# Optimization experiments

Hardware: AMD Instinct MI355X
Metric: run time of the kernel (lower is better)

The kernel has to match this reference:

```python
import jax, jax.numpy as jnp
import numpy as np

N = 100000   # nodes
E = 1600000  # edges (avg degree 16)
D = 64       # feature dim
STEPS = 3

def setup_inputs() -> dict:
    key = jax.random.key(0)
    ks = jax.random.split(key, 16)
    def rn(i, shape, scale=1.0):
        return jax.random.normal(ks[i], shape, dtype=jnp.float32) * scale
    inp = {
        "nodes": rn(0, (N, D)),
        "edges": rn(1, (E, D)),
        "globals_": rn(2, (1, D)),
        "senders": jax.random.randint(ks[3], (E,), 0, N, dtype=jnp.int32),
        "receivers": jax.random.randint(ks[4], (E,), 0, N, dtype=jnp.int32),
        # edge MLP: in 4*D -> D -> D
        "We1": rn(5, (4 * D, D), (4 * D) ** -0.5),
        "be1": jnp.zeros((D,), jnp.float32),
        "We2": rn(6, (D, D), D ** -0.5),
        "be2": jnp.zeros((D,), jnp.float32),
        # node MLP: in 3*D -> D -> D
        "Wn1": rn(7, (3 * D, D), (3 * D) ** -0.5),
        "bn1": jnp.zeros((D,), jnp.float32),
        "Wn2": rn(8, (D, D), D ** -0.5),
        "bn2": jnp.zeros((D,), jnp.float32),
        # global MLP: in 3*D -> D -> D
        "Wg1": rn(9, (3 * D, D), (3 * D) ** -0.5),
        "bg1": jnp.zeros((D,), jnp.float32),
        "Wg2": rn(10, (D, D), D ** -0.5),
        "bg2": jnp.zeros((D,), jnp.float32),
    }
    return inp

def _mlp(x, W1, b1, W2, b2):
    return jax.nn.relu(x @ W1 + b1) @ W2 + b2

def reference(nodes, edges, globals_, senders, receivers,
              We1, be1, We2, be2, Wn1, bn1, Wn2, bn2, Wg1, bg1, Wg2, bg2):
    g = globals_  # [1, D], single graph
    n_nodes = nodes.shape[0]
    for _ in range(STEPS):
        # --- edge update: gather sender/receiver node feats + broadcast globals ---
        sent = nodes[senders]        # [E, D]
        recv = nodes[receivers]      # [E, D]
        ge = jnp.broadcast_to(g, (edges.shape[0], g.shape[-1]))
        edges = _mlp(jnp.concatenate([edges, sent, recv, ge], axis=-1),
                     We1, be1, We2, be2)  # [E, D]
        # --- aggregate edges to nodes (received messages) ---
        received = jax.ops.segment_sum(edges, receivers, num_segments=n_nodes)
        gn = jnp.broadcast_to(g, (n_nodes, g.shape[-1]))
        nodes = _mlp(jnp.concatenate([nodes, received, gn], axis=-1),
                     Wn1, bn1, Wn2, bn2)  # [N, D]
        # --- aggregate to globals (single graph => full sums) ---
        agg_n = jnp.sum(nodes, axis=0, keepdims=True)  # [1, D]
        agg_e = jnp.sum(edges, axis=0, keepdims=True)  # [1, D]
        g = _mlp(jnp.concatenate([agg_n, agg_e, g], axis=-1),
                 Wg1, bg1, Wg2, bg2)  # [1, D]
    return nodes, edges, g
```

## Files before the change

kernel.cpp:

```cpp
#include <hip/hip_runtime.h>

#define DD 64
typedef unsigned int uint32;
typedef unsigned short ushort16;
typedef short bf16x8 __attribute__((ext_vector_type(8)));
typedef float f32x4 __attribute__((ext_vector_type(4)));

__device__ __forceinline__ ushort16 f2bf(float x) {
    uint32 u = __float_as_uint(x);
    uint32 r = (u + 0x7FFFu + ((u >> 16) & 1u)) >> 16;
    return (ushort16)r;
}
__device__ __forceinline__ float bf2f(ushort16 h) {
    return __uint_as_float(((uint32)h) << 16);
}

__device__ __forceinline__ void split8f(const float4& a, const float4& b, bf16x8& ah, bf16x8& al) {
    float xs[8] = {a.x, a.y, a.z, a.w, b.x, b.y, b.z, b.w};
#pragma unroll
    for (int i = 0; i < 8; ++i) {
        ushort16 hi = f2bf(xs[i]);
        ah[i] = (short)hi;
        al[i] = (short)f2bf(xs[i] - bf2f(hi));
    }
}

__device__ __forceinline__ void mfma_ks(const unsigned short* __restrict__ wks, int l,
                                        const bf16x8* ah, const bf16x8* al, f32x4 (*acc)[4]) {
#pragma unroll
    for (int tt = 0; tt < 4; ++tt) {
        bf16x8 bh = *(const bf16x8*)(wks + ((size_t)(tt * 2 + 0) * 64 + l) * 8);
        bf16x8 bl = *(const bf16x8*)(wks + ((size_t)(tt * 2 + 1) * 64 + l) * 8);
#pragma unroll
        for (int m = 0; m < 4; ++m) {
            acc[m][tt] = __builtin_amdgcn_mfma_f32_16x16x32_bf16(ah[m], bh, acc[m][tt], 0, 0, 0);
            acc[m][tt] = __builtin_amdgcn_mfma_f32_16x16x32_bf16(ah[m], bl, acc[m][tt], 0, 0, 0);
            acc[m][tt] = __builtin_amdgcn_mfma_f32_16x16x32_bf16(al[m], bh, acc[m][tt], 0, 0, 0);
        }
    }
}
__device__ __forceinline__ void mfma_ks_hi(const unsigned short* __restrict__ wks, int l,
                                           const bf16x8* ah, f32x4 (*acc)[4]) {
#pragma unroll
    for (int tt = 0; tt < 4; ++tt) {
        bf16x8 bh = *(const bf16x8*)(wks + ((size_t)(tt * 2 + 0) * 64 + l) * 8);
        bf16x8 bl = *(const bf16x8*)(wks + ((size_t)(tt * 2 + 1) * 64 + l) * 8);
#pragma unroll
        for (int m = 0; m < 4; ++m) {
            acc[m][tt] = __builtin_amdgcn_mfma_f32_16x16x32_bf16(ah[m], bh, acc[m][tt], 0, 0, 0);
            acc[m][tt] = __builtin_amdgcn_mfma_f32_16x16x32_bf16(ah[m], bl, acc[m][tt], 0, 0, 0);
        }
    }
}
__device__ __forceinline__ void mfma_ks1(const unsigned short* __restrict__ wks, int l,
                                         bf16x8 ah, bf16x8 al, f32x4* acc) {
#pragma unroll
    for (int tt = 0; tt < 4; ++tt) {
        bf16x8 bh = *(const bf16x8*)(wks + ((size_t)(tt * 2 + 0) * 64 + l) * 8);
        bf16x8 bl = *(const bf16x8*)(wks + ((size_t)(tt * 2 + 1) * 64 + l) * 8);
        acc[tt] = __builtin_amdgcn_mfma_f32_16x16x32_bf16(ah, bh, acc[tt], 0, 0, 0);
        acc[tt] = __builtin_amdgcn_mfma_f32_16x16x32_bf16(ah, bl, acc[tt], 0, 0, 0);
        acc[tt] = __builtin_amdgcn_mfma_f32_16x16x32_bf16(al, bh, acc[tt], 0, 0, 0);
    }
}

__global__ void zero_counts_kernel(int* __restrict__ counts, int N) {
    int i = blockIdx.x * blockDim.x + threadIdx.x;
    if (i < N) counts[i] = 0;
}
__global__ void hist_kernel(const int* __restrict__ recv, int* __restrict__ counts, int E) {
    int i = blockIdx.x * blockDim.x + threadIdx.x;
    if (i < E) atomicAdd(&counts[recv[i]], 1);
}
__global__ __launch_bounds__(1024) void scan_kernel(const int* __restrict__ counts,
                                                    int* __restrict__ offs,
                                                    int* __restrict__ cursor, int N) {
    __shared__ int sm[1024];
    __shared__ int carryS;
    int t = threadIdx.x;
    if (t == 0) carryS = 0;
    __syncthreads();
    for (int base = 0; base < N; base += 4096) {
        int idx = base + t * 4;
        int x0 = (idx + 0 < N) ? counts[idx + 0] : 0;
        int x1 = (idx + 1 < N) ? counts[idx + 1] : 0;
        int x2 = (idx + 2 < N) ? counts[idx + 2] : 0;
        int x3 = (idx + 3 < N) ? counts[idx + 3] : 0;
        int s1 = x0 + x1, s2 = s1 + x2, s3 = s2 + x3;
        sm[t] = s3;
        __syncthreads();
        for (int d = 1; d < 1024; d <<= 1) {
            int v = (t >= d) ? sm[t - d] : 0;
            __syncthreads();
            sm[t] += v;
            __syncthreads();
        }
        int excl = sm[t] - s3 + carryS;
        if (idx < N)     { offs[idx]     = excl;      cursor[idx]     = excl; }
        if (idx + 1 < N) { offs[idx + 1] = excl + x0; cursor[idx + 1] = excl + x0; }
        if (idx + 2 < N) { offs[idx + 2] = excl + s1; cursor[idx + 2] = excl + s1; }
        if (idx + 3 < N) { offs[idx + 3] = excl + s2; cursor[idx + 3] = excl + s2; }
        int chunkTotal = sm[1023];
        __syncthreads();
        if (t == 0) carryS += chunkTotal;
        __syncthreads();
    }
    if (t == 0) offs[N] = carryS;
}
__global__ void scatter_kernel(const int* __restrict__ recv, int* __restrict__ cursor,
                               int* __restrict__ perm, int* __restrict__ inv, int E) {
    int i = blockIdx.x * blockDim.x + threadIdx.x;
    if (i < E) {
        int p = atomicAdd(&cursor[recv[i]], 1);
        perm[p] = i;
        inv[i] = p;
    }
}

__global__ void prep_bias_kernel(const float* __restrict__ g,
                                 const float* __restrict__ We1, const float* __restrict__ be1,
                                 const float* __restrict__ Wn1, const float* __restrict__ bn1,
                                 float* __restrict__ be1e, float* __restrict__ bn1e) {
    int j = threadIdx.x;
    float a = be1[j];
    float b = bn1[j];
    for (int k = 0; k < DD; ++k) {
        float gk = g[k];
        a = fmaf(gk, We1[(192 + k) * DD + j], a);
        b = fmaf(gk, Wn1[(128 + k) * DD + j], b);
    }
    be1e[j] = a;
    bn1e[j] = b;
}

__global__ void prep_nodes_kernel(const float* __restrict__ src,
                                  unsigned short* __restrict__ h, unsigned short* __restrict__ l,
                                  int total) {
    int i = blockIdx.x * blockDim.x + threadIdx.x;
    if (i < total) {
        float x = src[i];
        ushort16 hi = f2bf(x);
        h[i] = hi;
        l[i] = f2bf(x - bf2f(hi));
    }
}

__global__ void prep_edges_kernel(const float* __restrict__ e0, const int* __restrict__ inv,
                                  unsigned short* __restrict__ ebf, int E) {
    int tid = blockIdx.x * blockDim.x + threadIdx.x;
    if (tid < E * 8) {
        int e = tid >> 3, part = tid & 7;
        const float* p = e0 + (size_t)e * DD + part * 8;
        float4 a = *(const float4*)(p);
        float4 b = *(const float4*)(p + 4);
        uint4 o;
        o.x = (uint32)f2bf(a.x) | ((uint32)f2bf(a.y) << 16);
        o.y = (uint32)f2bf(a.z) | ((uint32)f2bf(a.w) << 16);
        o.z = (uint32)f2bf(b.x) | ((uint32)f2bf(b.y) << 16);
        o.w = (uint32)f2bf(b.z) | ((uint32)f2bf(b.w) << 16);
        int ip = inv[e];
        *(uint4*)(ebf + (size_t)ip * DD + part * 8) = o;
    }
}

__device__ __forceinline__ void prep_pack(const float* __restrict__ W, int nks,
                                          unsigned short* __restrict__ dst, int tid) {
    if (tid < nks * 2048) {
        int i = tid & 7, lane = (tid >> 3) & 63, tt = (tid >> 9) & 3, ks = tid >> 11;
        int k = ks * 32 + (lane >> 4) * 8 + i;
        int n = tt * 16 + (lane & 15);
        float x = W[k * DD + n];
        ushort16 hi = f2bf(x);
        ushort16 lo = f2bf(x - bf2f(hi));
        dst[(((ks * 4 + tt) * 2 + 0) * 64 + lane) * 8 + i] = hi;
        dst[(((ks * 4 + tt) * 2 + 1) * 64 + lane) * 8 + i] = lo;
    }
}
__global__ void prep_weights_kernel(const float* __restrict__ We1, const float* __restrict__ We2,
                                    const float* __restrict__ Wn1, const float* __restrict__ Wn2,
                                    unsigned short* __restrict__ we1p, unsigned short* __restrict__ we2p,
                                    unsigned short* __restrict__ wn1p, unsigned short* __restrict__ wn2p) {
    int tid = blockIdx.x * blockDim.x + threadIdx.x;
    prep_pack(We1, 6, we1p, tid);
    prep_pack(We2, 2, we2p, tid);
    prep_pack(Wn1, 4, wn1p, tid);
    prep_pack(Wn2, 2, wn2p, tid);
}

template<int IN_BF, int OUT_F32>
__global__ __launch_bounds__(256, 3) void edge_kernel_t(
    const float* __restrict__ edges_f32, const unsigned short* __restrict__ edges_bf,
    const unsigned short* __restrict__ nodes_h, const unsigned short* __restrict__ nodes_l,
    const int* __restrict__ senders, const int* __restrict__ receivers,
    const int* __restrict__ perm,
    const unsigned short* __restrict__ w1, const float* __restrict__ b1,
    const unsigned short* __restrict__ w2, const float* __restrict__ b2,
    float* __restrict__ eout_f32, unsigned short* __restrict__ eout_bf,
    float* __restrict__ received, float* __restrict__ agg_e, int E)
{
    __shared__ int PE[4][64];
    __shared__ int SID[4][64];
    __shared__ int RID[4][64];
    __shared__ float PS[4][64];
    __shared__ __align__(16) char HB[4][4096];

    const int t = threadIdx.x;
    const int w = t >> 6, l = t & 63;
    const int lm = l & 15, kq = l >> 4;
    const int base = (blockIdx.x << 8) + (w << 6);

    {
        int pos = base + l;
        int pe = perm[min(pos, E - 1)];
        PE[w][l] = pe;
        SID[w][l] = senders[pe];
        RID[w][l] = receivers[pe];
    }

    int pe_m[4], sid_m[4], rid_m[4];
#pragma unroll
    for (int m = 0; m < 4; ++m) {
        pe_m[m]  = PE[w][(m << 4) + lm];
        sid_m[m] = SID[w][(m << 4) + lm];
        rid_m[m] = RID[w][(m << 4) + lm];
    }

    uint4 rbe[4][2];
    float4 re[4][4];
    if (IN_BF) {
#pragma unroll
        for (int m = 0; m < 4; ++m) {
            int row = min(base + (m << 4) + lm, E - 1);
            const unsigned short* p = edges_bf + (size_t)row * DD + kq * 8;
            rbe[m][0] = *(const uint4*)(p);
            rbe[m][1] = *(const uint4*)(p + 32);
        }
    } else {
#pragma unroll
        for (int m = 0; m < 4; ++m) {
            const float* p = edges_f32 + (size_t)pe_m[m] * DD + kq * 8;
            re[m][0] = *(const float4*)(p);
            re[m][1] = *(const float4*)(p + 4);
            re[m][2] = *(const float4*)(p + 32);
            re[m][3] = *(const float4*)(p + 36);
        }
    }
    uint4 rsh[4][2];
#pragma unroll
    for (int m = 0; m < 4; ++m) {
        const unsigned short* p = nodes_h + (size_t)sid_m[m] * DD + kq * 8;
        rsh[m][0] = *(const uint4*)(p);
        rsh[m][1] = *(const uint4*)(p + 32);
    }
    uint4 rrh[4][2], rrl[4][2];
#pragma unroll
    for (int m = 0; m < 4; ++m) {
        const unsigned short* ph = nodes_h + (size_t)rid_m[m] * DD + kq * 8;
        const unsigned short* pl = nodes_l + (size_t)rid_m[m] * DD + kq * 8;
        rrh[m][0] = *(const uint4*)(ph);
        rrh[m][1] = *(const uint4*)(ph + 32);
        rrl[m][0] = *(const uint4*)(pl);
        rrl[m][1] = *(const uint4*)(pl + 32);
    }

    f32x4 acc[4][4];
#pragma unroll
    for (int tt = 0; tt < 4; ++tt) {
        float b = b1[tt * 16 + lm];
#pragma unroll
        for (int m = 0; m < 4; ++m) { acc[m][tt][0] = b; acc[m][tt][1] = b; acc[m][tt][2] = b; acc[m][tt][3] = b; }
    }

    if (IN_BF) {
#pragma unroll
        for (int ks2 = 0; ks2 < 2; ++ks2) {
            bf16x8 ah[4];
#pragma unroll
            for (int m = 0; m < 4; ++m) ah[m] = *(bf16x8*)&rbe[m][ks2];
            mfma_ks_hi(w1 + (size_t)ks2 * 4096, l, ah, acc);
        }
    } else {
#pragma unroll
        for (int ks2 = 0; ks2 < 2; ++ks2) {
            bf16x8 ah[4], al[4];
#pragma unroll
            for (int m = 0; m < 4; ++m) split8f(re[m][ks2 * 2], re[m][ks2 * 2 + 1], ah[m], al[m]);
            mfma_ks(w1 + (size_t)ks2 * 4096, l, ah, al, acc);
        }
    }
#pragma unroll
    for (int ks2 = 0; ks2 < 2; ++ks2) {
        bf16x8 ah[4];
#pragma unroll
        for (int m = 0; m < 4; ++m) ah[m] = *(bf16x8*)&rsh[m][ks2];
        mfma_ks_hi(w1 + (size_t)(2 + ks2) * 4096, l, ah, acc);
    }
#pragma unroll
    for (int ks2 = 0; ks2 < 2; ++ks2) {
        bf16x8 ah[4], al[4];
#pragma unroll
        for (int m = 0; m < 4; ++m) { ah[m] = *(bf16x8*)&rrh[m][ks2]; al[m] = *(bf16x8*)&rrl[m][ks2]; }
        mfma_ks(w1 + (size_t)(4 + ks2) * 4096, l, ah, al, acc);
    }

    float b2v[4];
#pragma unroll
    for (int tt = 0; tt < 4; ++tt) b2v[tt] = b2[tt * 16 + lm];
    float sreg[4] = {0.f, 0.f, 0.f, 0.f};
    char* hh = &HB[w][0];
    char* hl = &HB[w][2048];

#pragma unroll
    for (int m = 0; m < 4; ++m) {
#pragma unroll
        for (int tt = 0; tt < 4; ++tt)
#pragma unroll
            for (int r = 0; r < 4; ++r) {
                int row = (kq << 2) + r;
                int col = (tt << 4) + lm;
                float hv = fmaxf(acc[m][tt][r], 0.f);
                ushort16 hi = f2bf(hv);
                ushort16 lo = f2bf(hv - bf2f(hi));
                int boff = (row << 7) + ((((col >> 3) ^ (row & 7)) & 7) << 4) + ((col & 7) << 1);
                *(unsigned short*)(hh + boff) = hi;
                *(unsigned short*)(hl + boff) = lo;
            }

        f32x4 acc2[4];
#pragma unroll
        for (int tt = 0; tt < 4; ++tt) { acc2[tt][0] = b2v[tt]; acc2[tt][1] = b2v[tt]; acc2[tt][2] = b2v[tt]; acc2[tt][3] = b2v[tt]; }
#pragma unroll
        for (int ks = 0; ks < 2; ++ks) {
            int boff = (lm << 7) + ((((kq + ks * 4) ^ (lm & 7)) & 7) << 4);
            bf16x8 ah = *(const bf16x8*)(hh + boff);
            bf16x8 al = *(const bf16x8*)(hl + boff);
            mfma_ks1(w2 + (size_t)ks * 4096, l, ah, al, acc2);
        }

#pragma unroll
        for (int tt = 0; tt < 4; ++tt)
#pragma unroll
            for (int r = 0; r < 4; ++r) {
                int rowp = base + (m << 4) + (kq << 2) + r;
                if (rowp < E) sreg[tt] += acc2[tt][r];
            }

#pragma unroll
        for (int tt = 0; tt < 4; ++tt)
#pragma unroll
            for (int r = 0; r < 4; ++r) {
                int row = (kq << 2) + r;
                int col = (tt << 4) + lm;
                int boff = (row << 8) + ((((col >> 2) ^ (row & 15)) & 15) << 4) + ((col & 3) << 2);
                *(float*)(&HB[w][0] + boff) = acc2[tt][r];
            }

        {
            int rowp = base + (m << 4) + lm;
            float4 vv[4];
#pragma unroll
            for (int jj = 0; jj < 4; ++jj) {
                int slot = (4 * kq + jj) ^ (lm & 15);
                vv[jj] = *(float4*)(&HB[w][0] + (lm << 8) + (slot << 4));
            }
            if (rowp < E) {
                if (OUT_F32) {
                    float4* dst = (float4*)(eout_f32 + (size_t)pe_m[m] * DD);
#pragma unroll
                    for (int jj = 0; jj < 4; ++jj) dst[kq * 4 + jj] = vv[jj];
                } else {
                    uint4 o0, o1;
                    o0.x = (uint32)f2bf(vv[0].x) | ((uint32)f2bf(vv[0].y) << 16);
                    o0.y = (uint32)f2bf(vv[0].z) | ((uint32)f2bf(vv[0].w) << 16);
                    o0.z = (uint32)f2bf(vv[1].x) | ((uint32)f2bf(vv[1].y) << 16);
                    o0.w = (uint32)f2bf(vv[1].z) | ((uint32)f2bf(vv[1].w) << 16);
                    o1.x = (uint32)f2bf(vv[2].x) | ((uint32)f2bf(vv[2].y) << 16);
                    o1.y = (uint32)f2bf(vv[2].z) | ((uint32)f2bf(vv[2].w) << 16);
                    o1.z = (uint32)f2bf(vv[3].x) | ((uint32)f2bf(vv[3].y) << 16);
                    o1.w = (uint32)f2bf(vv[3].z) | ((uint32)f2bf(vv[3].w) << 16);
                    unsigned short* dst = eout_bf + (size_t)rowp * DD + kq * 16;
                    *(uint4*)(dst) = o0;
                    *(uint4*)(dst + 8) = o1;
                }
            }
        }

        {
            float run = 0.f;
#pragma unroll
            for (int r = 0; r < 16; ++r) {
                int rowp = base + (m << 4) + r;
                if (rowp < E) {
                    int boff = (r << 8) + ((((l >> 2) ^ (r & 15)) & 15) << 4) + ((l & 3) << 2);
                    float v = *(const float*)(&HB[w][0] + boff);
                    int rid = RID[w][(m << 4) + r];
                    run += v;
                    bool flush;
                    if (r == 15) flush = true;
                    else flush = (rowp + 1 >= E) || (RID[w][(m << 4) + r + 1] != rid);
                    if (flush) {
                        atomicAdd(&received[(size_t)rid * DD + l], run);
                        run = 0.f;
                    }
                }
            }
        }
    }

#pragma unroll
    for (int tt = 0; tt < 4; ++tt) {
        float s = sreg[tt];
        s += __shfl_xor(s, 16, 64);
        s += __shfl_xor(s, 32, 64);
        if (l < 16) PS[w][tt * 16 + l] = s;
    }
    __syncthreads();
    if (t < 64) {
        float s = PS[0][t] + PS[1][t] + PS[2][t] + PS[3][t];
        atomicAdd(agg_e + t, s);
    }
}

__global__ __launch_bounds__(256, 2) void node_kernel_mfma(
    const unsigned short* __restrict__ nodes_h_in, const unsigned short* __restrict__ nodes_l_in,
    const float* __restrict__ received,
    const unsigned short* __restrict__ w1, const float* __restrict__ b1,
    const unsigned short* __restrict__ w2, const float* __restrict__ b2,
    float* __restrict__ nodes_out,
    unsigned short* __restrict__ nodes_h_out, unsigned short* __restrict__ nodes_l_out,
    int write_pk, float* __restrict__ agg_n, int N)
{
    __shared__ unsigned short HB[4][4][2][1024];
    __shared__ float PS[4][64];

    const int t = threadIdx.x;
    const int w = t >> 6, l = t & 63;
    const int lm = l & 15, kq = l >> 4;
    const int base = (blockIdx.x << 8) + (w << 6);

    int gi[4];
#pragma unroll
    for (int m = 0; m < 4; ++m) gi[m] = min(base + (m << 4) + lm, N - 1);

    uint4 rnh[4][2], rnl[4][2];
#pragma unroll
    for (int m = 0; m < 4; ++m) {
        const unsigned short* ph = nodes_h_in + (size_t)gi[m] * DD + kq * 8;
        const unsigned short* pl = nodes_l_in + (size_t)gi[m] * DD + kq * 8;
        rnh[m][0] = *(const uint4*)(ph);
        rnh[m][1] = *(const uint4*)(ph + 32);
        rnl[m][0] = *(const uint4*)(pl);
        rnl[m][1] = *(const uint4*)(pl + 32);
    }
    float4 rc[4][4];
#pragma unroll
    for (int m = 0; m < 4; ++m) {
        const float* p = received + (size_t)gi[m] * DD + kq * 8;
        rc[m][0] = *(const float4*)(p);
        rc[m][1] = *(const float4*)(p + 4);
        rc[m][2] = *(const float4*)(p + 32);
        rc[m][3] = *(const float4*)(p + 36);
    }

    f32x4 acc[4][4];
#pragma unroll
    for (int tt = 0; tt < 4; ++tt) {
        float b = b1[tt * 16 + lm];
#pragma unroll
        for (int m = 0; m < 4; ++m) { acc[m][tt][0] = b; acc[m][tt][1] = b; acc[m][tt][2] = b; acc[m][tt][3] = b; }
    }

#pragma unroll
    for (int ks2 = 0; ks2 < 2; ++ks2) {
        bf16x8 ah[4], al[4];
#pragma unroll
        for (int m = 0; m < 4; ++m) { ah[m] = *(bf16x8*)&rnh[m][ks2]; al[m] = *(bf16x8*)&rnl[m][ks2]; }
        mfma_ks(w1 + (size_t)ks2 * 4096, l, ah, al, acc);
    }
#pragma unroll
    for (int ks2 = 0; ks2 < 2; ++ks2) {
        bf16x8 ah[4], al[4];
#pragma unroll
        for (int m = 0; m < 4; ++m) split8f(rc[m][ks2 * 2], rc[m][ks2 * 2 + 1], ah[m], al[m]);
        mfma_ks(w1 + (size_t)(2 + ks2) * 4096, l, ah, al, acc);
    }

#pragma unroll
    for (int m = 0; m < 4; ++m) {
        char* hh = (char*)&HB[w][m][0][0];
        char* hl = (char*)&HB[w][m][1][0];
#pragma unroll
        for (int tt = 0; tt < 4; ++tt)
#pragma unroll
            for (int r = 0; r < 4; ++r) {
                int row = (kq << 2) + r;
                int col = (tt << 4) + lm;
                float hv = fmaxf(acc[m][tt][r], 0.f);
                ushort16 hi = f2bf(hv);
                ushort16 lo = f2bf(hv - bf2f(hi));
                int boff = (row << 7) + ((((col >> 3) ^ (row & 7)) & 7) << 4) + ((col & 7) << 1);
                *(unsigned short*)(hh + boff) = hi;
                *(unsigned short*)(hl + boff) = lo;
            }
    }

    f32x4 acc2[4][4];
#pragma unroll
    for (int tt = 0; tt < 4; ++tt) {
        float b = b2[tt * 16 + lm];
#pragma unroll
        for (int m = 0; m < 4; ++m) { acc2[m][tt][0] = b; acc2[m][tt][1] = b; acc2[m][tt][2] = b; acc2[m][tt][3] = b; }
    }
#pragma unroll
    for (int ks = 0; ks < 2; ++ks) {
        bf16x8 ah[4], al[4];
#pragma unroll
        for (int m = 0; m < 4; ++m) {
            int boff = (lm << 7) + ((((kq + ks * 4) ^ (lm & 7)) & 7) << 4);
            ah[m] = *(const bf16x8*)((char*)&HB[w][m][0][0] + boff);
            al[m] = *(const bf16x8*)((char*)&HB[w][m][1][0] + boff);
        }
        mfma_ks(w2 + (size_t)ks * 4096, l, ah, al, acc2);
    }

#pragma unroll
    for (int tt = 0; tt < 4; ++tt) {
        float s = 0.f;
#pragma unroll
        for (int m = 0; m < 4; ++m)
#pragma unroll
            for (int r = 0; r < 4; ++r) {
                int rowg = base + (m << 4) + (kq << 2) + r;
                if (rowg < N) s += acc2[m][tt][r];
            }
        s += __shfl_xor(s, 16, 64);
        s += __shfl_xor(s, 32, 64);
        if (l < 16) PS[w][tt * 16 + l] = s;
    }

    char* CW = (char*)&HB[w][0][0][0];
#pragma unroll
    for (int m = 0; m < 4; ++m)
#pragma unroll
        for (int tt = 0; tt < 4; ++tt)
#pragma unroll
            for (int r = 0; r < 4; ++r) {
                int row = (kq << 2) + r;
                int col = (tt << 4) + lm;
                int boff = (row << 8) + ((((col >> 2) ^ (row & 15)) & 15) << 4) + ((col & 3) << 2);
                *(float*)(CW + m * 4096 + boff) = acc2[m][tt][r];
            }
#pragma unroll
    for (int m = 0; m < 4; ++m) {
        int rowg = base + (m << 4) + lm;
        float4 vv[4];
#pragma unroll
        for (int jj = 0; jj < 4; ++jj) {
            int slot = (4 * kq + jj) ^ (lm & 15);
            vv[jj] = *(float4*)(CW + m * 4096 + (lm << 8) + (slot << 4));
        }
        if (rowg < N) {
            float4* dst = (float4*)(nodes_out + (size_t)rowg * DD);
#pragma unroll
            for (int jj = 0; jj < 4; ++jj) dst[kq * 4 + jj] = vv[jj];
            if (write_pk) {
                unsigned short* hdst = nodes_h_out + (size_t)rowg * DD + kq * 16;
                unsigned short* ldst = nodes_l_out + (size_t)rowg * DD + kq * 16;
                uint4 oh, ol;
                float xs[16] = {vv[0].x, vv[0].y, vv[0].z, vv[0].w,
                                vv[1].x, vv[1].y, vv[1].z, vv[1].w,
                                vv[2].x, vv[2].y, vv[2].z, vv[2].w,
                                vv[3].x, vv[3].y, vv[3].z, vv[3].w};
                uint32 hw[8], lw[8];
#pragma unroll
                for (int q = 0; q < 8; ++q) {
                    ushort16 h0 = f2bf(xs[2 * q]);
                    ushort16 h1 = f2bf(xs[2 * q + 1]);
                    ushort16 l0 = f2bf(xs[2 * q] - bf2f(h0));
                    ushort16 l1 = f2bf(xs[2 * q + 1] - bf2f(h1));
                    hw[q] = (uint32)h0 | ((uint32)h1 << 16);
                    lw[q] = (uint32)l0 | ((uint32)l1 << 16);
                }
                oh.x = hw[0]; oh.y = hw[1]; oh.z = hw[2]; oh.w = hw[3];
                *(uint4*)(hdst) = oh;
                oh.x = hw[4]; oh.y = hw[5]; oh.z = hw[6]; oh.w = hw[7];
                *(uint4*)(hdst + 8) = oh;
                ol.x = lw[0]; ol.y = lw[1]; ol.z = lw[2]; ol.w = lw[3];
                *(uint4*)(ldst) = ol;
                ol.x = lw[4]; ol.y = lw[5]; ol.z = lw[6]; ol.w = lw[7];
                *(uint4*)(ldst + 8) = ol;
            }
        }
    }

    __syncthreads();
    if (t < 64) {
        float s = PS[0][t] + PS[1][t] + PS[2][t] + PS[3][t];
        atomicAdd(agg_n + t, s);
    }
}

__global__ void global_kernel(const float* __restrict__ agg_n, const float* __restrict__ agg_e,
                              const float* __restrict__ g_in,
                              const float* __restrict__ Wg1, const float* __restrict__ bg1,
                              const float* __restrict__ Wg2, const float* __restrict__ bg2,
                              float* __restrict__ g_out)
{
    __shared__ float h[64];
    int j = threadIdx.x;
    float a = bg1[j];
    for (int k = 0; k < DD; ++k) a = fmaf(agg_n[k], Wg1[k * DD + j], a);
    for (int k = 0; k < DD; ++k) a = fmaf(agg_e[k], Wg1[(64 + k) * DD + j], a);
    for (int k = 0; k < DD; ++k) a = fmaf(g_in[k],  Wg1[(128 + k) * DD + j], a);
    h[j] = fmaxf(a, 0.f);
    __syncthreads();
    float o = bg2[j];
    for (int k = 0; k < DD; ++k) o = fmaf(h[k], Wg2[k * DD + j], o);
    g_out[j] = o;
}

extern "C" void kernel_launch(void* const* d_in, const int* in_sizes, int n_in,
                              void* d_out, int out_size, void* d_ws, size_t ws_size,
                              hipStream_t stream) {
    const float* nodes0 = (const float*)d_in[0];
    const float* edges0 = (const float*)d_in[1];
    const float* g0     = (const float*)d_in[2];
    const int* senders   = (const int*)d_in[3];
    const int* receivers = (const int*)d_in[4];
    const float* We1 = (const float*)d_in[5];
    const float* be1 = (const float*)d_in[6];
    const float* We2 = (const float*)d_in[7];
    const float* be2 = (const float*)d_in[8];
    const float* Wn1 = (const float*)d_in[9];
    const float* bn1 = (const float*)d_in[10];
    const float* Wn2 = (const float*)d_in[11];
    const float* bn2 = (const float*)d_in[12];
    const float* Wg1 = (const float*)d_in[13];
    const float* bg1 = (const float*)d_in[14];
    const float* Wg2 = (const float*)d_in[15];
    const float* bg2 = (const float*)d_in[16];

    const int N = in_sizes[0] / DD;
    const int E = in_sizes[1] / DD;

    float* out_nodes = (float*)d_out;
    float* out_edges = out_nodes + (size_t)N * DD;
    float* out_g     = out_edges + (size_t)E * DD;

    float* ws = (float*)d_ws;
    float* received = ws;
    float* aggs = received + (size_t)N * DD;
    float* agg_n = aggs;
    float* agg_e = aggs + 64;
    float* b1e   = aggs + 128;
    float* b1n   = aggs + 192;
    float* g1    = aggs + 256;
    float* g2    = aggs + 320;
    int* counts = (int*)(aggs + 512);
    int* offs   = counts + N;
    int* cursor = offs + N + 4;
    int* perm   = cursor + N;
    int* inv    = perm + E;
    unsigned short* nodes_h = (unsigned short*)(inv + E);
    unsigned short* nodes_l = nodes_h + (size_t)N * DD;
    unsigned short* we1p = nodes_l + (size_t)N * DD;
    unsigned short* we2p = we1p + 24576;
    unsigned short* wn1p = we2p + 8192;
    unsigned short* wn2p = wn1p + 16384;
    unsigned short* edges_bf = wn2p + 8192;

    size_t need = (size_t)((char*)(edges_bf + (size_t)E * DD) - (char*)d_ws);
    const bool use_bf = (ws_size >= need);

    const int eblocks = (E + 255) / 256;
    const int nblocks = (N + 255) / 256;

    zero_counts_kernel<<<(N + 255) / 256, 256, 0, stream>>>(counts, N);
    hist_kernel<<<(E + 255) / 256, 256, 0, stream>>>(receivers, counts, E);
    scan_kernel<<<1, 1024, 0, stream>>>(counts, offs, cursor, N);
    scatter_kernel<<<(E + 255) / 256, 256, 0, stream>>>(receivers, cursor, perm, inv, E);
    prep_weights_kernel<<<48, 256, 0, stream>>>(We1, We2, Wn1, Wn2, we1p, we2p, wn1p, wn2p);
    prep_nodes_kernel<<<(N * DD + 255) / 256, 256, 0, stream>>>(nodes0, nodes_h, nodes_l, N * DD);
    if (use_bf)
        prep_edges_kernel<<<(E * 8 + 255) / 256, 256, 0, stream>>>(edges0, inv, edges_bf, E);

    for (int s = 0; s < 3; ++s) {
        const float* esrc_f32 = (s == 0) ? edges0 : out_edges;
        const float* gin  = (s == 0) ? g0 : ((s == 1) ? g1 : g2);
        float* gout       = (s == 2) ? out_g : ((s == 0) ? g1 : g2);

        hipMemsetAsync(received, 0, ((size_t)N * DD + 128) * sizeof(float), stream);
        prep_bias_kernel<<<1, 64, 0, stream>>>(gin, We1, be1, Wn1, bn1, b1e, b1n);

        if (use_bf) {
            if (s == 2)
                edge_kernel_t<1, 1><<<eblocks, 256, 0, stream>>>(esrc_f32, edges_bf, nodes_h, nodes_l,
                    senders, receivers, perm, we1p, b1e, we2p, be2,
                    out_edges, edges_bf, received, agg_e, E);
            else
                edge_kernel_t<1, 0><<<eblocks, 256, 0, stream>>>(esrc_f32, edges_bf, nodes_h, nodes_l,
                    senders, receivers, perm, we1p, b1e, we2p, be2,
                    out_edges, edges_bf, received, agg_e, E);
        } else {
            edge_kernel_t<0, 1><<<eblocks, 256, 0, stream>>>(esrc_f32, edges_bf, nodes_h, nodes_l,
                senders, receivers, perm, we1p, b1e, we2p, be2,
                out_edges, edges_bf, received, agg_e, E);
        }

        node_kernel_mfma<<<nblocks, 256, 0, stream>>>(nodes_h, nodes_l, received,
                                                      wn1p, b1n, wn2p, bn2,
                                                      out_nodes, nodes_h, nodes_l,
                                                      (s < 2) ? 1 : 0, agg_n, N);
        global_kernel<<<1, 64, 0, stream>>>(agg_n, agg_e, gin, Wg1, bg1, Wg2, bg2, gout);
    }
}
```

Baseline: 1.918 ms.

## Pre-scatter sender node features into edge-order buffer to replace random gathers

Builds a sender-sorted CSR (histogram, scan, scatter) that maps each sender to its edge slots in receiver-sorted order. A new kernel then writes each node's bf16 high part into a contiguous per-edge buffer after every node update, so the edge kernel reads sender features sequentially instead of gathering them at random. Receiver ids are also precomputed in permuted order, and the segmented-sum run now carries across 16-row groups, cutting atomics. This adds about 200MB of extra writes per step plus a larger workspace requirement, trading random reads for streaming writes.

```diff
diff --git a/kernel.cpp b/kernel.cpp
--- a/kernel.cpp
+++ b/kernel.cpp
@@ -68,9 +68,9 @@
     int i = blockIdx.x * blockDim.x + threadIdx.x;
     if (i < N) counts[i] = 0;
 }
-__global__ void hist_kernel(const int* __restrict__ recv, int* __restrict__ counts, int E) {
+__global__ void hist_kernel(const int* __restrict__ idx, int* __restrict__ counts, int E) {
     int i = blockIdx.x * blockDim.x + threadIdx.x;
-    if (i < E) atomicAdd(&counts[recv[i]], 1);
+    if (i < E) atomicAdd(&counts[idx[i]], 1);
 }
 __global__ __launch_bounds__(1024) void scan_kernel(const int* __restrict__ counts,
                                                     int* __restrict__ offs,
@@ -116,6 +116,35 @@
         inv[i] = p;
     }
 }
+__global__ void scatter2_kernel(const int* __restrict__ send, int* __restrict__ cursor,
+                                const int* __restrict__ inv, int* __restrict__ dslot, int E) {
+    int i = blockIdx.x * blockDim.x + threadIdx.x;
+    if (i < E) {
+        int p = atomicAdd(&cursor[send[i]], 1);
+        dslot[p] = inv[i];
+    }
+}
+__global__ void ridperm_kernel(const int* __restrict__ recv, const int* __restrict__ perm,
+                               int* __restrict__ ridp, int E) {
+    int i = blockIdx.x * blockDim.x + threadIdx.x;
+    if (i < E) ridp[i] = recv[perm[i]];
+}
+
+__global__ __launch_bounds__(256) void sender_scatter_kernel(
+    const unsigned short* __restrict__ nodes_h, const int* __restrict__ soffs,
+    const int* __restrict__ dslot, unsigned short* __restrict__ esg, int N)
+{
+    int gid = blockIdx.x * blockDim.x + threadIdx.x;
+    int n = gid >> 4, c = gid & 15;
+    if (n < N) {
+        uint2 v = *(const uint2*)(nodes_h + (size_t)n * DD + c * 4);
+        int s0 = soffs[n], s1 = soffs[n + 1];
+        for (int j = s0; j < s1; ++j) {
+            int slot = dslot[j];
+            *(uint2*)(esg + (size_t)slot * DD + c * 4) = v;
+        }
+    }
+}
 
 __global__ void prep_bias_kernel(const float* __restrict__ g,
                                  const float* __restrict__ We1, const float* __restrict__ be1,
@@ -187,12 +216,13 @@
     prep_pack(Wn2, 2, wn2p, tid);
 }
 
-template<int IN_BF, int OUT_F32>
+template<int IN_BF, int OUT_F32, int SG>
 __global__ __launch_bounds__(256, 3) void edge_kernel_t(
     const float* __restrict__ edges_f32, const unsigned short* __restrict__ edges_bf,
+    const unsigned short* __restrict__ esg,
     const unsigned short* __restrict__ nodes_h, const unsigned short* __restrict__ nodes_l,
     const int* __restrict__ senders, const int* __restrict__ receivers,
-    const int* __restrict__ perm,
+    const int* __restrict__ ridp, const int* __restrict__ perm,
     const unsigned short* __restrict__ w1, const float* __restrict__ b1,
     const unsigned short* __restrict__ w2, const float* __restrict__ b2,
     float* __restrict__ eout_f32, unsigned short* __restrict__ eout_bf,
@@ -210,19 +240,24 @@
     const int base = (blockIdx.x << 8) + (w << 6);
 
     {
-        int pos = base + l;
-        int pe = perm[min(pos, E - 1)];
-        PE[w][l] = pe;
-        SID[w][l] = senders[pe];
-        RID[w][l] = receivers[pe];
+        int pos = min(base + l, E - 1);
+        if (SG) {
+            RID[w][l] = ridp[pos];
+            if (OUT_F32) PE[w][l] = perm[pos];
+        } else {
+            int pe = perm[pos];
+            PE[w][l] = pe;
+            SID[w][l] = senders[pe];
+            RID[w][l] = receivers[pe];
+        }
     }
 
     int pe_m[4], sid_m[4], rid_m[4];
 #pragma unroll
     for (int m = 0; m < 4; ++m) {
-        pe_m[m]  = PE[w][(m << 4) + lm];
-        sid_m[m] = SID[w][(m << 4) + lm];
         rid_m[m] = RID[w][(m << 4) + lm];
+        if (OUT_F32 || !IN_BF || !SG) pe_m[m] = PE[w][(m << 4) + lm];
+        if (!SG) sid_m[m] = SID[w][(m << 4) + lm];
     }
 
     uint4 rbe[4][2];
@@ -246,11 +281,21 @@
         }
     }
     uint4 rsh[4][2];
-#pragma unroll
-    for (int m = 0; m < 4; ++m) {
-        const unsigned short* p = nodes_h + (size_t)sid_m[m] * DD + kq * 8;
-        rsh[m][0] = *(const uint4*)(p);
-        rsh[m][1] = *(const uint4*)(p + 32);
+    if (SG) {
+#pragma unroll
+        for (int m = 0; m < 4; ++m) {
+            int row = min(base + (m << 4) + lm, E - 1);
+            const unsigned short* p = esg + (size_t)row * DD + kq * 8;
+            rsh[m][0] = *(const uint4*)(p);
+            rsh[m][1] = *(const uint4*)(p + 32);
+        }
+    } else {
+#pragma unroll
+        for (int m = 0; m < 4; ++m) {
+            const unsigned short* p = nodes_h + (size_t)sid_m[m] * DD + kq * 8;
+            rsh[m][0] = *(const uint4*)(p);
+            rsh[m][1] = *(const uint4*)(p + 32);
+        }
     }
     uint4 rrh[4][2], rrl[4][2];
 #pragma unroll
@@ -307,6 +352,7 @@
 #pragma unroll
     for (int tt = 0; tt < 4; ++tt) b2v[tt] = b2[tt * 16 + lm];
     float sreg[4] = {0.f, 0.f, 0.f, 0.f};
+    float run = 0.f;
     char* hh = &HB[w][0];
     char* hl = &HB[w][2048];
 
@@ -386,18 +432,18 @@
         }
 
         {
-            float run = 0.f;
 #pragma unroll
             for (int r = 0; r < 16; ++r) {
-                int rowp = base + (m << 4) + r;
+                int wr = (m << 4) + r;
+                int rowp = base + wr;
                 if (rowp < E) {
                     int boff = (r << 8) + ((((l >> 2) ^ (r & 15)) & 15) << 4) + ((l & 3) << 2);
                     float v = *(const float*)(&HB[w][0] + boff);
-                    int rid = RID[w][(m << 4) + r];
+                    int rid = RID[w][wr];
                     run += v;
                     bool flush;
-                    if (r == 15) flush = true;
-                    else flush = (rowp + 1 >= E) || (RID[w][(m << 4) + r + 1] != rid);
+                    if (wr == 63) flush = true;
+                    else flush = (rowp + 1 >= E) || (RID[w][wr + 1] != rid);
                     if (flush) {
                         atomicAdd(&received[(size_t)rid * DD + l], run);
                         run = 0.f;
@@ -668,9 +714,17 @@
     unsigned short* wn1p = we2p + 8192;
     unsigned short* wn2p = wn1p + 16384;
     unsigned short* edges_bf = wn2p + 8192;
-
-    size_t need = (size_t)((char*)(edges_bf + (size_t)E * DD) - (char*)d_ws);
-    const bool use_bf = (ws_size >= need);
+    int* ridp    = (int*)(edges_bf + (size_t)E * DD);
+    int* counts2 = ridp + E;
+    int* offs2   = counts2 + N;
+    int* cursor2 = offs2 + N + 4;
+    int* dslot   = cursor2 + N;
+    unsigned short* esg = (unsigned short*)(dslot + E);
+
+    size_t need_bf = (size_t)((char*)ridp - (char*)d_ws);
+    size_t need_sg = (size_t)((char*)(esg + (size_t)E * DD) - (char*)d_ws);
+    const bool use_bf = (ws_size >= need_bf);
+    const bool use_sg = (ws_size >= need_sg);
 
     const int eblocks = (E + 255) / 256;
     const int nblocks = (N + 255) / 256;
@@ -683,6 +737,14 @@
     prep_nodes_kernel<<<(N * DD + 255) / 256, 256, 0, stream>>>(nodes0, nodes_h, nodes_l, N * DD);
     if (use_bf)
         prep_edges_kernel<<<(E * 8 + 255) / 256, 256, 0, stream>>>(edges0, inv, edges_bf, E);
+    if (use_sg) {
+        ridperm_kernel<<<(E + 255) / 256, 256, 0, stream>>>(receivers, perm, ridp, E);
+        zero_counts_kernel<<<(N + 255) / 256, 256, 0, stream>>>(counts2, N);
+        hist_kernel<<<(E + 255) / 256, 256, 0, stream>>>(senders, counts2, E);
+        scan_kernel<<<1, 1024, 0, stream>>>(counts2, offs2, cursor2, N);
+        scatter2_kernel<<<(E + 255) / 256, 256, 0, stream>>>(senders, cursor2, inv, dslot, E);
+        sender_scatter_kernel<<<(N * 16 + 255) / 256, 256, 0, stream>>>(nodes_h, offs2, dslot, esg, N);
+    }
 
     for (int s = 0; s < 3; ++s) {
         const float* esrc_f32 = (s == 0) ? edges0 : out_edges;
@@ -692,18 +754,27 @@
         hipMemsetAsync(received, 0, ((size_t)N * DD + 128) * sizeof(float), stream);
         prep_bias_kernel<<<1, 64, 0, stream>>>(gin, We1, be1, Wn1, bn1, b1e, b1n);
 
-        if (use_bf) {
+        if (use_sg) {
             if (s == 2)
-                edge_kernel_t<1, 1><<<eblocks, 256, 0, stream>>>(esrc_f32, edges_bf, nodes_h, nodes_l,
-                    senders, receivers, perm, we1p, b1e, we2p, be2,
+                edge_kernel_t<1, 1, 1><<<eblocks, 256, 0, stream>>>(esrc_f32, edges_bf, esg,
+                    nodes_h, nodes_l, senders, receivers, ridp, perm, we1p, b1e, we2p, be2,
                     out_edges, edges_bf, received, agg_e, E);
             else
-                edge_kernel_t<1, 0><<<eblocks, 256, 0, stream>>>(esrc_f32, edges_bf, nodes_h, nodes_l,
-                    senders, receivers, perm, we1p, b1e, we2p, be2,
+                edge_kernel_t<1, 0, 1><<<eblocks, 256, 0, stream>>>(esrc_f32, edges_bf, esg,
+                    nodes_h, nodes_l, senders, receivers, ridp, perm, we1p, b1e, we2p, be2,
+                    out_edges, edges_bf, received, agg_e, E);
+        } else if (use_bf) {
+            if (s == 2)
+                edge_kernel_t<1, 1, 0><<<eblocks, 256, 0, stream>>>(esrc_f32, edges_bf, esg,
+                    nodes_h, nodes_l, senders, receivers, ridp, perm, we1p, b1e, we2p, be2,
+                    out_edges, edges_bf, received, agg_e, E);
+            else
+                edge_kernel_t<1, 0, 0><<<eblocks, 256, 0, stream>>>(esrc_f32, edges_bf, esg,
+                    nodes_h, nodes_l, senders, receivers, ridp, perm, we1p, b1e, we2p, be2,
                     out_edges, edges_bf, received, agg_e, E);
         } else {
-            edge_kernel_t<0, 1><<<eblocks, 256, 0, stream>>>(esrc_f32, edges_bf, nodes_h, nodes_l,
-                senders, receivers, perm, we1p, b1e, we2p, be2,
+            edge_kernel_t<0, 1, 0><<<eblocks, 256, 0, stream>>>(esrc_f32, edges_bf, esg,
+                nodes_h, nodes_l, senders, receivers, ridp, perm, we1p, b1e, we2p, be2,
                 out_edges, edges_bf, received, agg_e, E);
         }
 
@@ -711,6 +782,8 @@
                                                       wn1p, b1n, wn2p, bn2,
                                                       out_nodes, nodes_h, nodes_l,
                                                       (s < 2) ? 1 : 0, agg_n, N);
+        if (use_sg && s < 2)
+            sender_scatter_kernel<<<(N * 16 + 255) / 256, 256, 0, stream>>>(nodes_h, offs2, dslot, esg, N);
         global_kernel<<<1, 64, 0, stream>>>(agg_n, agg_e, gin, Wg1, bg1, Wg2, bg2, gout);
     }
 }
```

Measured after the change: 2.578 ms. 1.34x slower.

## Drop low-bf16 split for receiver features and hidden layer, pre-permute indices

Applied to the files above, without the earlier changes.

The edge kernel no longer loads the low bf16 half of receiver node features or splits the hidden activations into hi/lo, so fewer MFMAs run and fewer gathers are issued. Sender/receiver indices are pre-permuted once into sorted order, removing the perm-indirected index lookups in each step. The running segment-sum now carries across 16-row groups within a wave, cutting atomics, and the occupancy hint rises to 4 blocks. The cost is lower numerical precision in the edge MLP, plus an extra setup kernel and workspace.

```diff
diff --git a/kernel.cpp b/kernel.cpp
--- a/kernel.cpp
+++ b/kernel.cpp
@@ -63,14 +63,24 @@
         acc[tt] = __builtin_amdgcn_mfma_f32_16x16x32_bf16(al, bh, acc[tt], 0, 0, 0);
     }
 }
+__device__ __forceinline__ void mfma_ks1_hi(const unsigned short* __restrict__ wks, int l,
+                                            bf16x8 ah, f32x4* acc) {
+#pragma unroll
+    for (int tt = 0; tt < 4; ++tt) {
+        bf16x8 bh = *(const bf16x8*)(wks + ((size_t)(tt * 2 + 0) * 64 + l) * 8);
+        bf16x8 bl = *(const bf16x8*)(wks + ((size_t)(tt * 2 + 1) * 64 + l) * 8);
+        acc[tt] = __builtin_amdgcn_mfma_f32_16x16x32_bf16(ah, bh, acc[tt], 0, 0, 0);
+        acc[tt] = __builtin_amdgcn_mfma_f32_16x16x32_bf16(ah, bl, acc[tt], 0, 0, 0);
+    }
+}
 
 __global__ void zero_counts_kernel(int* __restrict__ counts, int N) {
     int i = blockIdx.x * blockDim.x + threadIdx.x;
     if (i < N) counts[i] = 0;
 }
-__global__ void hist_kernel(const int* __restrict__ recv, int* __restrict__ counts, int E) {
+__global__ void hist_kernel(const int* __restrict__ idx, int* __restrict__ counts, int E) {
     int i = blockIdx.x * blockDim.x + threadIdx.x;
-    if (i < E) atomicAdd(&counts[recv[i]], 1);
+    if (i < E) atomicAdd(&counts[idx[i]], 1);
 }
 __global__ __launch_bounds__(1024) void scan_kernel(const int* __restrict__ counts,
                                                     int* __restrict__ offs,
@@ -116,6 +126,16 @@
         inv[i] = p;
     }
 }
+__global__ void idxperm_kernel(const int* __restrict__ recv, const int* __restrict__ send,
+                               const int* __restrict__ perm,
+                               int* __restrict__ ridp, int* __restrict__ sidp, int E) {
+    int i = blockIdx.x * blockDim.x + threadIdx.x;
+    if (i < E) {
+        int pe = perm[i];
+        ridp[i] = recv[pe];
+        sidp[i] = send[pe];
+    }
+}
 
 __global__ void prep_bias_kernel(const float* __restrict__ g,
                                  const float* __restrict__ We1, const float* __restrict__ be1,
@@ -188,19 +208,19 @@
 }
 
 template<int IN_BF, int OUT_F32>
-__global__ __launch_bounds__(256, 3) void edge_kernel_t(
+__global__ __launch_bounds__(256, 4) void edge_kernel_t(
     const float* __restrict__ edges_f32, const unsigned short* __restrict__ edges_bf,
-    const unsigned short* __restrict__ nodes_h, const unsigned short* __restrict__ nodes_l,
+    const unsigned short* __restrict__ nodes_h,
     const int* __restrict__ senders, const int* __restrict__ receivers,
+    const int* __restrict__ ridp, const int* __restrict__ sidp,
     const int* __restrict__ perm,
     const unsigned short* __restrict__ w1, const float* __restrict__ b1,
     const unsigned short* __restrict__ w2, const float* __restrict__ b2,
     float* __restrict__ eout_f32, unsigned short* __restrict__ eout_bf,
     float* __restrict__ received, float* __restrict__ agg_e, int E)
 {
+    __shared__ int RID[4][64];
     __shared__ int PE[4][64];
-    __shared__ int SID[4][64];
-    __shared__ int RID[4][64];
     __shared__ float PS[4][64];
     __shared__ __align__(16) char HB[4][4096];
 
@@ -210,19 +230,30 @@
     const int base = (blockIdx.x << 8) + (w << 6);
 
     {
-        int pos = base + l;
-        int pe = perm[min(pos, E - 1)];
-        PE[w][l] = pe;
-        SID[w][l] = senders[pe];
-        RID[w][l] = receivers[pe];
-    }
-
-    int pe_m[4], sid_m[4], rid_m[4];
-#pragma unroll
-    for (int m = 0; m < 4; ++m) {
-        pe_m[m]  = PE[w][(m << 4) + lm];
-        sid_m[m] = SID[w][(m << 4) + lm];
+        int pos = min(base + l, E - 1);
+        if (IN_BF) {
+            RID[w][l] = ridp[pos];
+            if (OUT_F32) PE[w][l] = perm[pos];
+        } else {
+            int pe = perm[pos];
+            PE[w][l] = pe;
+            RID[w][l] = receivers[pe];
+        }
+    }
+
+    int sid_m[4];
+#pragma unroll
+    for (int m = 0; m < 4; ++m) {
+        int pos = min(base + (m << 4) + lm, E - 1);
+        if (IN_BF) sid_m[m] = sidp[pos];
+    }
+    int pe_m[4];
+    int rid_m[4];
+#pragma unroll
+    for (int m = 0; m < 4; ++m) {
         rid_m[m] = RID[w][(m << 4) + lm];
+        if (OUT_F32 || !IN_BF) pe_m[m] = PE[w][(m << 4) + lm];
+        if (!IN_BF) sid_m[m] = senders[pe_m[m]];
     }
 
     uint4 rbe[4][2];
@@ -252,15 +283,12 @@
         rsh[m][0] = *(const uint4*)(p);
         rsh[m][1] = *(const uint4*)(p + 32);
     }
-    uint4 rrh[4][2], rrl[4][2];
+    uint4 rrh[4][2];
 #pragma unroll
     for (int m = 0; m < 4; ++m) {
         const unsigned short* ph = nodes_h + (size_t)rid_m[m] * DD + kq * 8;
-        const unsigned short* pl = nodes_l + (size_t)rid_m[m] * DD + kq * 8;
         rrh[m][0] = *(const uint4*)(ph);
         rrh[m][1] = *(const uint4*)(ph + 32);
-        rrl[m][0] = *(const uint4*)(pl);
-        rrl[m][1] = *(const uint4*)(pl + 32);
     }
 
     f32x4 acc[4][4];
@@ -297,18 +325,18 @@
     }
 #pragma unroll
     for (int ks2 = 0; ks2 < 2; ++ks2) {
-        bf16x8 ah[4], al[4];
-#pragma unroll
-        for (int m = 0; m < 4; ++m) { ah[m] = *(bf16x8*)&rrh[m][ks2]; al[m] = *(bf16x8*)&rrl[m][ks2]; }
-        mfma_ks(w1 + (size_t)(4 + ks2) * 4096, l, ah, al, acc);
+        bf16x8 ah[4];
+#pragma unroll
+        for (int m = 0; m < 4; ++m) ah[m] = *(bf16x8*)&rrh[m][ks2];
+        mfma_ks_hi(w1 + (size_t)(4 + ks2) * 4096, l, ah, acc);
     }
 
     float b2v[4];
 #pragma unroll
     for (int tt = 0; tt < 4; ++tt) b2v[tt] = b2[tt * 16 + lm];
     float sreg[4] = {0.f, 0.f, 0.f, 0.f};
+    float run = 0.f;
     char* hh = &HB[w][0];
-    char* hl = &HB[w][2048];
 
 #pragma unroll
     for (int m = 0; m < 4; ++m) {
@@ -319,11 +347,8 @@
                 int row = (kq << 2) + r;
                 int col = (tt << 4) + lm;
                 float hv = fmaxf(acc[m][tt][r], 0.f);
-                ushort16 hi = f2bf(hv);
-                ushort16 lo = f2bf(hv - bf2f(hi));
                 int boff = (row << 7) + ((((col >> 3) ^ (row & 7)) & 7) << 4) + ((col & 7) << 1);
-                *(unsigned short*)(hh + boff) = hi;
-                *(unsigned short*)(hl + boff) = lo;
+                *(unsigned short*)(hh + boff) = f2bf(hv);
             }
 
         f32x4 acc2[4];
@@ -333,8 +358,7 @@
         for (int ks = 0; ks < 2; ++ks) {
             int boff = (lm << 7) + ((((kq + ks * 4) ^ (lm & 7)) & 7) << 4);
             bf16x8 ah = *(const bf16x8*)(hh + boff);
-            bf16x8 al = *(const bf16x8*)(hl + boff);
-            mfma_ks1(w2 + (size_t)ks * 4096, l, ah, al, acc2);
+            mfma_ks1_hi(w2 + (size_t)ks * 4096, l, ah, acc2);
         }
 
 #pragma unroll
@@ -386,18 +410,18 @@
         }
 
         {
-            float run = 0.f;
 #pragma unroll
             for (int r = 0; r < 16; ++r) {
-                int rowp = base + (m << 4) + r;
+                int wr = (m << 4) + r;
+                int rowp = base + wr;
                 if (rowp < E) {
                     int boff = (r << 8) + ((((l >> 2) ^ (r & 15)) & 15) << 4) + ((l & 3) << 2);
                     float v = *(const float*)(&HB[w][0] + boff);
-                    int rid = RID[w][(m << 4) + r];
+                    int rid = RID[w][wr];
                     run += v;
                     bool flush;
-                    if (r == 15) flush = true;
-                    else flush = (rowp + 1 >= E) || (RID[w][(m << 4) + r + 1] != rid);
+                    if (wr == 63) flush = true;
+                    else flush = (rowp + 1 >= E) || (RID[w][wr + 1] != rid);
                     if (flush) {
                         atomicAdd(&received[(size_t)rid * DD + l], run);
                         run = 0.f;
@@ -661,7 +685,9 @@
     int* cursor = offs + N + 4;
     int* perm   = cursor + N;
     int* inv    = perm + E;
-    unsigned short* nodes_h = (unsigned short*)(inv + E);
+    int* ridp   = inv + E;
+    int* sidp   = ridp + E;
+    unsigned short* nodes_h = (unsigned short*)(sidp + E);
     unsigned short* nodes_l = nodes_h + (size_t)N * DD;
     unsigned short* we1p = nodes_l + (size_t)N * DD;
     unsigned short* we2p = we1p + 24576;
@@ -669,8 +695,8 @@
     unsigned short* wn2p = wn1p + 16384;
     unsigned short* edges_bf = wn2p + 8192;
 
-    size_t need = (size_t)((char*)(edges_bf + (size_t)E * DD) - (char*)d_ws);
-    const bool use_bf = (ws_size >= need);
+    size_t need_bf = (size_t)((char*)(edges_bf + (size_t)E * DD) - (char*)d_ws);
+    const bool use_bf = (ws_size >= need_bf);
 
     const int eblocks = (E + 255) / 256;
     const int nblocks = (N + 255) / 256;
@@ -681,8 +707,10 @@
     scatter_kernel<<<(E + 255) / 256, 256, 0, stream>>>(receivers, cursor, perm, inv, E);
     prep_weights_kernel<<<48, 256, 0, stream>>>(We1, We2, Wn1, Wn2, we1p, we2p, wn1p, wn2p);
     prep_nodes_kernel<<<(N * DD + 255) / 256, 256, 0, stream>>>(nodes0, nodes_h, nodes_l, N * DD);
-    if (use_bf)
+    if (use_bf) {
+        idxperm_kernel<<<(E + 255) / 256, 256, 0, stream>>>(receivers, senders, perm, ridp, sidp, E);
         prep_edges_kernel<<<(E * 8 + 255) / 256, 256, 0, stream>>>(edges0, inv, edges_bf, E);
+    }
 
     for (int s = 0; s < 3; ++s) {
         const float* esrc_f32 = (s == 0) ? edges0 : out_edges;
@@ -694,16 +722,16 @@
 
         if (use_bf) {
             if (s == 2)
-                edge_kernel_t<1, 1><<<eblocks, 256, 0, stream>>>(esrc_f32, edges_bf, nodes_h, nodes_l,
-                    senders, receivers, perm, we1p, b1e, we2p, be2,
+                edge_kernel_t<1, 1><<<eblocks, 256, 0, stream>>>(esrc_f32, edges_bf, nodes_h,
+                    senders, receivers, ridp, sidp, perm, we1p, b1e, we2p, be2,
                     out_edges, edges_bf, received, agg_e, E);
             else
-                edge_kernel_t<1, 0><<<eblocks, 256, 0, stream>>>(esrc_f32, edges_bf, nodes_h, nodes_l,
-                    senders, receivers, perm, we1p, b1e, we2p, be2,
+                edge_kernel_t<1, 0><<<eblocks, 256, 0, stream>>>(esrc_f32, edges_bf, nodes_h,
+                    senders, receivers, ridp, sidp, perm, we1p, b1e, we2p, be2,
                     out_edges, edges_bf, received, agg_e, E);
         } else {
-            edge_kernel_t<0, 1><<<eblocks, 256, 0, stream>>>(esrc_f32, edges_bf, nodes_h, nodes_l,
-                senders, receivers, perm, we1p, b1e, we2p, be2,
+            edge_kernel_t<0, 1><<<eblocks, 256, 0, stream>>>(esrc_f32, edges_bf, nodes_h,
+                senders, receivers, ridp, sidp, perm, we1p, b1e, we2p, be2,
                 out_edges, edges_bf, received, agg_e, E);
         }
 
```

After: 2.315 ms. 20.7% more time.
